# Optimization experiments

Hardware: AMD Instinct MI355X
Metric: run time of the kernel (lower is better)

## Reference

```python
import jax, jax.numpy as jnp
import numpy as np
from jax import lax

GUARD_CELLS = 80
BG_CELLS = 80
ALPHA = 1.8
CFAR_UNITS = 1 + 2 * GUARD_CELLS + 2 * BG_CELLS          # 321
GUARD_UNITS = 2 * GUARD_CELLS + 1                         # 161
BG_AREA = CFAR_UNITS ** 2 - GUARD_UNITS ** 2              # background ring cell count
FRONT_DIV = (GUARD_UNITS ** 2) * ALPHA


def box_sum(x, k):
    """Same-padded KxK box sum over NCHW x (C=1), via separable 1D convs.

    Mathematically identical to a Conv2d with all-ones KxK kernel, zero bias,
    padding (k-1)//2 -- but O(N*K) instead of O(N*K^2).
    """
    p = (k - 1) // 2
    kh = jnp.ones((1, 1, k, 1), x.dtype)  # OIHW
    kw = jnp.ones((1, 1, 1, k), x.dtype)
    y = lax.conv_general_dilated(x, kh, window_strides=(1, 1), padding=[(p, p), (0, 0)])
    y = lax.conv_general_dilated(y, kw, window_strides=(1, 1), padding=[(0, 0), (p, p)])
    return y


def setup_inputs() -> dict:
    key = jax.random.key(0)
    x = jax.random.uniform(key, (4, 1, 1024, 1024), dtype=jnp.float32)
    return {"x": x}


def reference(x) -> jnp.ndarray:
    allsum = box_sum(x, CFAR_UNITS)            # conv1: 321x321 ones box
    front = box_sum(x, GUARD_UNITS)            # conv2: 161x161 ones box
    back = (allsum - front) / jnp.float32(BG_AREA)     # div1: 1x1 conv = scale
    front = front / jnp.float32(FRONT_DIV)             # div2: 1x1 conv = scale
    return front / back
```

## Files before the change

### kernel.cpp

```cpp
#include <hip/hip_runtime.h>
#include <hip/hip_bf16.h>


#define IMG 4
#define H 1024
#define W 1024
#define SEGR 8
#define NSEG 128
#define PADL 164
#define PADR 164
#define ROWLEN (PADL + W + PADR)

__global__ __launch_bounds__(256, 4) void hbv_kernel(const float* __restrict__ x,
                                                     float* __restrict__ g161,
                                                     float* __restrict__ g321,
                                                     float* __restrict__ Btot) {
    __shared__ float P[4][ROWLEN];
    __shared__ float Hx[4][W];
    const int wave = threadIdx.x >> 6;
    const int lane = threadIdx.x & 63;
    const int q    = threadIdx.x;
    const int blk  = blockIdx.x;
    const size_t rowbase = (size_t)blk << 3;

    float4 acc1 = make_float4(0.f, 0.f, 0.f, 0.f);
    float4 acc3 = make_float4(0.f, 0.f, 0.f, 0.f);

#pragma unroll
    for (int ch = 0; ch < 2; ++ch) {
        const size_t row = rowbase + (ch << 2) + wave;
        {
            const float4* xr = reinterpret_cast<const float4*>(x + row * W);
            float v[16];
            float4 a0 = xr[(lane << 2) + 0];
            float4 a1 = xr[(lane << 2) + 1];
            float4 a2 = xr[(lane << 2) + 2];
            float4 a3 = xr[(lane << 2) + 3];
            v[0]=a0.x; v[1]=a0.y; v[2]=a0.z; v[3]=a0.w;
            v[4]=a1.x; v[5]=a1.y; v[6]=a1.z; v[7]=a1.w;
            v[8]=a2.x; v[9]=a2.y; v[10]=a2.z; v[11]=a2.w;
            v[12]=a3.x; v[13]=a3.y; v[14]=a3.z; v[15]=a3.w;
            float s = 0.f;
#pragma unroll
            for (int j = 0; j < 16; ++j) { s += v[j]; v[j] = s; }
            float t = s;
#pragma unroll
            for (int d = 1; d < 64; d <<= 1) {
                float u = __shfl_up(t, d, 64);
                if (lane >= d) t += u;
            }
            const float off = t - s;
#pragma unroll
            for (int j = 0; j < 16; ++j) v[j] += off;
            const float tot = __shfl(t, 63, 64);

            float* rowP = P[wave];
            float4* Pr = reinterpret_cast<float4*>(rowP + PADL);
            Pr[(lane << 2) + 0] = make_float4(v[0], v[1], v[2], v[3]);
            Pr[(lane << 2) + 1] = make_float4(v[4], v[5], v[6], v[7]);
            Pr[(lane << 2) + 2] = make_float4(v[8], v[9], v[10], v[11]);
            Pr[(lane << 2) + 3] = make_float4(v[12], v[13], v[14], v[15]);
            float4* Pz = reinterpret_cast<float4*>(rowP);
            if (lane < 41) {
                Pz[lane]       = make_float4(0.f, 0.f, 0.f, 0.f);
                Pz[297 + lane] = make_float4(tot, tot, tot, tot);
            }
        }
        const float* Pw = &P[wave][PADL];

#pragma unroll
        for (int k = 0; k < 16; ++k) {
            const int c = lane + (k << 6);
            Hx[wave][c] = Pw[c + 80] - Pw[c - 81];
        }
        __syncthreads();
        {
            float* o = g161 + (rowbase + (ch << 2)) * W;
            const float4* Hf = reinterpret_cast<const float4*>(Hx);
#pragma unroll
            for (int r = 0; r < 4; ++r) {
                float4 h = Hf[(r << 8) + q];
                acc1.x += h.x; acc1.y += h.y; acc1.z += h.z; acc1.w += h.w;
                reinterpret_cast<float4*>(o + (size_t)r * W)[q] = acc1;
            }
        }
        __syncthreads();
#pragma unroll
        for (int k = 0; k < 16; ++k) {
            const int c = lane + (k << 6);
            Hx[wave][c] = Pw[c + 160] - Pw[c - 161];
        }
        __syncthreads();
        {
            float* o = g321 + (rowbase + (ch << 2)) * W;
            const float4* Hf = reinterpret_cast<const float4*>(Hx);
#pragma unroll
            for (int r = 0; r < 4; ++r) {
                float4 h = Hf[(r << 8) + q];
                acc3.x += h.x; acc3.y += h.y; acc3.z += h.z; acc3.w += h.w;
                reinterpret_cast<float4*>(o + (size_t)r * W)[q] = acc3;
            }
        }
        __syncthreads();
    }

    const int img = blk >> 7;
    const int seg = blk & 127;
    float4* bt = reinterpret_cast<float4*>(Btot);
    bt[((size_t)img << 15)         + (seg << 8) + q] = acc1;
    bt[((size_t)(IMG + img) << 15) + (seg << 8) + q] = acc3;
}

__global__ __launch_bounds__(256) void segscan_kernel(const float* __restrict__ Btot,
                                                      float* __restrict__ SP) {
    __shared__ float T[4][64];
    const int wave = threadIdx.x >> 6;
    const int lane = threadIdx.x & 63;
    const int bi   = blockIdx.x >> 4;
    const int col  = ((blockIdx.x & 15) << 6) + lane;
    const size_t base = ((size_t)bi << 17) + ((size_t)(wave << 5) << 10) + col;

    float v[32];
#pragma unroll
    for (int s = 0; s < 32; ++s) v[s] = Btot[base + ((size_t)s << 10)];
    float run = 0.f;
#pragma unroll
    for (int s = 0; s < 32; ++s) { const float t = v[s]; v[s] = run; run += t; }
    T[wave][lane] = run;
    __syncthreads();
    float off = 0.f;
    for (int w = 0; w < wave; ++w) off += T[w][lane];
#pragma unroll
    for (int s = 0; s < 32; ++s) SP[base + ((size_t)s << 10)] = v[s] + off;
}

__global__ __launch_bounds__(512) void final_kernel(const float* __restrict__ g161,
                                                    const float* __restrict__ g321,
                                                    const float* __restrict__ SP,
                                                    float* __restrict__ out) {
    const int img = blockIdx.x >> 9;
    const int r   = ((blockIdx.x & 511) << 1) + (threadIdx.x >> 8);
    const int c4  = threadIdx.x & 255;

    const float4* P1 = reinterpret_cast<const float4*>(g161 + ((size_t)img << 20));
    const float4* P3 = reinterpret_cast<const float4*>(g321 + ((size_t)img << 20));
    const float4* SP1 = reinterpret_cast<const float4*>(SP) + ((size_t)img << 15);
    const float4* SP3 = reinterpret_cast<const float4*>(SP) + ((size_t)(IMG + img) << 15);

    const int hi1 = min(r + 80, H - 1),  lo1 = r - 81;
    const int hi3 = min(r + 160, H - 1), lo3 = r - 161;

    float4 f  = P1[((size_t)hi1 << 8) + c4];
    float4 fs = SP1[(((size_t)hi1 >> 3) << 8) + c4];
    float fx = f.x + fs.x, fy = f.y + fs.y, fz = f.z + fs.z, fw = f.w + fs.w;
    if (lo1 >= 0) {
        float4 g  = P1[((size_t)lo1 << 8) + c4];
        float4 gs = SP1[(((size_t)lo1 >> 3) << 8) + c4];
        fx -= g.x + gs.x; fy -= g.y + gs.y; fz -= g.z + gs.z; fw -= g.w + gs.w;
    }
    float4 a  = P3[((size_t)hi3 << 8) + c4];
    float4 as = SP3[(((size_t)hi3 >> 3) << 8) + c4];
    float ax = a.x + as.x, ay = a.y + as.y, az = a.z + as.z, aw = a.w + as.w;
    if (lo3 >= 0) {
        float4 g  = P3[((size_t)lo3 << 8) + c4];
        float4 gs = SP3[(((size_t)lo3 >> 3) << 8) + c4];
        ax -= g.x + gs.x; ay -= g.y + gs.y; az -= g.z + gs.z; aw -= g.w + gs.w;
    }

    const float SCALE = (float)(77120.0 / 46657.8);
    float4 o;
    o.x = SCALE * fx * __builtin_amdgcn_rcpf(ax - fx);
    o.y = SCALE * fy * __builtin_amdgcn_rcpf(ay - fy);
    o.z = SCALE * fz * __builtin_amdgcn_rcpf(az - fz);
    o.w = SCALE * fw * __builtin_amdgcn_rcpf(aw - fw);
    reinterpret_cast<float4*>(out + ((size_t)img << 20) + ((size_t)r << 10))[c4] = o;
}

extern "C" void kernel_launch(void* const* d_in, const int* in_sizes, int n_in,
                              void* d_out, int out_size, void* d_ws, size_t ws_size,
                              hipStream_t stream) {
    const float* x = (const float*)d_in[0];
    float* outp = (float*)d_out;
    float* g161 = (float*)d_ws;
    float* g321 = g161 + (size_t)IMG * H * W;
    float* Btot = g321 + (size_t)IMG * H * W;
    float* SPb  = Btot + (size_t)2 * IMG * NSEG * W;

    hbv_kernel<<<dim3(IMG * NSEG), dim3(256), 0, stream>>>(x, g161, g321, Btot);
    segscan_kernel<<<dim3(128), dim3(256), 0, stream>>>(Btot, SPb);
    final_kernel<<<dim3(IMG * (H / 2)), dim3(512), 0, stream>>>(g161, g321, SPb, outp);
}
```

Baseline: 90.37 us.

## Shrink row segments to 4 and fuse horizontal diff with vertical accumulation

Each block now handles 4 rows instead of 8, giving 1024 blocks. Each thread reads the prefix rows straight from shared memory and accumulates both box widths in one pass, which removes the Hx staging buffer and most of the barriers. The segment scan now covers twice as many segments with 64 values per thread and writes its result back into Btot in place, dropping the separate SP buffer. In exchange the scan kernel does more work and uses more registers, global stores become scalar rather than float4, and the shared-memory reads are unaligned scalar loads.

```diff
diff --git a/kernel.cpp b/kernel.cpp
--- a/kernel.cpp
+++ b/kernel.cpp
@@ -5,133 +5,111 @@
 #define IMG 4
 #define H 1024
 #define W 1024
-#define SEGR 8
-#define NSEG 128
+#define SEGR 4
+#define NSEG 256
 #define PADL 164
 #define PADR 164
 #define ROWLEN (PADL + W + PADR)
 
-__global__ __launch_bounds__(256, 4) void hbv_kernel(const float* __restrict__ x,
-                                                     float* __restrict__ g161,
-                                                     float* __restrict__ g321,
-                                                     float* __restrict__ Btot) {
+__global__ __launch_bounds__(256) void hbv_kernel(const float* __restrict__ x,
+                                                  float* __restrict__ g161,
+                                                  float* __restrict__ g321,
+                                                  float* __restrict__ Btot) {
     __shared__ float P[4][ROWLEN];
-    __shared__ float Hx[4][W];
     const int wave = threadIdx.x >> 6;
     const int lane = threadIdx.x & 63;
-    const int q    = threadIdx.x;
+    const int tid  = threadIdx.x;
     const int blk  = blockIdx.x;
-    const size_t rowbase = (size_t)blk << 3;
+    const size_t rowbase = (size_t)blk << 2;
 
-    float4 acc1 = make_float4(0.f, 0.f, 0.f, 0.f);
-    float4 acc3 = make_float4(0.f, 0.f, 0.f, 0.f);
+    {
+        const size_t row = rowbase + wave;
+        const float4* xr = reinterpret_cast<const float4*>(x + row * W);
+        float v[16];
+        float4 a0 = xr[(lane << 2) + 0];
+        float4 a1 = xr[(lane << 2) + 1];
+        float4 a2 = xr[(lane << 2) + 2];
+        float4 a3 = xr[(lane << 2) + 3];
+        v[0]=a0.x; v[1]=a0.y; v[2]=a0.z; v[3]=a0.w;
+        v[4]=a1.x; v[5]=a1.y; v[6]=a1.z; v[7]=a1.w;
+        v[8]=a2.x; v[9]=a2.y; v[10]=a2.z; v[11]=a2.w;
+        v[12]=a3.x; v[13]=a3.y; v[14]=a3.z; v[15]=a3.w;
+        float s = 0.f;
+#pragma unroll
+        for (int j = 0; j < 16; ++j) { s += v[j]; v[j] = s; }
+        float t = s;
+#pragma unroll
+        for (int d = 1; d < 64; d <<= 1) {
+            float u = __shfl_up(t, d, 64);
+            if (lane >= d) t += u;
+        }
+        const float off = t - s;
+#pragma unroll
+        for (int j = 0; j < 16; ++j) v[j] += off;
+        const float tot = __shfl(t, 63, 64);
 
+        float* rowP = P[wave];
+        float4* Pr = reinterpret_cast<float4*>(rowP + PADL);
+        Pr[(lane << 2) + 0] = make_float4(v[0], v[1], v[2], v[3]);
+        Pr[(lane << 2) + 1] = make_float4(v[4], v[5], v[6], v[7]);
+        Pr[(lane << 2) + 2] = make_float4(v[8], v[9], v[10], v[11]);
+        Pr[(lane << 2) + 3] = make_float4(v[12], v[13], v[14], v[15]);
+        float4* Pz = reinterpret_cast<float4*>(rowP);
+        if (lane < 41) {
+            Pz[lane]       = make_float4(0.f, 0.f, 0.f, 0.f);
+            Pz[297 + lane] = make_float4(tot, tot, tot, tot);
+        }
+    }
+    __syncthreads();
+
+    float acc1[4] = {0.f, 0.f, 0.f, 0.f};
+    float acc3[4] = {0.f, 0.f, 0.f, 0.f};
 #pragma unroll
-    for (int ch = 0; ch < 2; ++ch) {
-        const size_t row = rowbase + (ch << 2) + wave;
-        {
-            const float4* xr = reinterpret_cast<const float4*>(x + row * W);
-            float v[16];
-            float4 a0 = xr[(lane << 2) + 0];
-            float4 a1 = xr[(lane << 2) + 1];
-            float4 a2 = xr[(lane << 2) + 2];
-            float4 a3 = xr[(lane << 2) + 3];
-            v[0]=a0.x; v[1]=a0.y; v[2]=a0.z; v[3]=a0.w;
-            v[4]=a1.x; v[5]=a1.y; v[6]=a1.z; v[7]=a1.w;
-            v[8]=a2.x; v[9]=a2.y; v[10]=a2.z; v[11]=a2.w;
-            v[12]=a3.x; v[13]=a3.y; v[14]=a3.z; v[15]=a3.w;
-            float s = 0.f;
+    for (int rr = 0; rr < SEGR; ++rr) {
+        const float* Pr = &P[rr][PADL];
+        float* o1 = g161 + (rowbase + rr) * W;
+        float* o3 = g321 + (rowbase + rr) * W;
 #pragma unroll
-            for (int j = 0; j < 16; ++j) { s += v[j]; v[j] = s; }
-            float t = s;
-#pragma unroll
-            for (int d = 1; d < 64; d <<= 1) {
-                float u = __shfl_up(t, d, 64);
-                if (lane >= d) t += u;
-            }
-            const float off = t - s;
-#pragma unroll
-            for (int j = 0; j < 16; ++j) v[j] += off;
-            const float tot = __shfl(t, 63, 64);
-
-            float* rowP = P[wave];
-            float4* Pr = reinterpret_cast<float4*>(rowP + PADL);
-            Pr[(lane << 2) + 0] = make_float4(v[0], v[1], v[2], v[3]);
-            Pr[(lane << 2) + 1] = make_float4(v[4], v[5], v[6], v[7]);
-            Pr[(lane << 2) + 2] = make_float4(v[8], v[9], v[10], v[11]);
-            Pr[(lane << 2) + 3] = make_float4(v[12], v[13], v[14], v[15]);
-            float4* Pz = reinterpret_cast<float4*>(rowP);
-            if (lane < 41) {
-                Pz[lane]       = make_float4(0.f, 0.f, 0.f, 0.f);
-                Pz[297 + lane] = make_float4(tot, tot, tot, tot);
-            }
+        for (int j = 0; j < 4; ++j) {
+            const int c = tid + (j << 8);
+            acc1[j] += Pr[c + 80]  - Pr[c - 81];
+            acc3[j] += Pr[c + 160] - Pr[c - 161];
+            o1[c] = acc1[j];
+            o3[c] = acc3[j];
         }
-        const float* Pw = &P[wave][PADL];
-
-#pragma unroll
-        for (int k = 0; k < 16; ++k) {
-            const int c = lane + (k << 6);
-            Hx[wave][c] = Pw[c + 80] - Pw[c - 81];
-        }
-        __syncthreads();
-        {
-            float* o = g161 + (rowbase + (ch << 2)) * W;
-            const float4* Hf = reinterpret_cast<const float4*>(Hx);
-#pragma unroll
-            for (int r = 0; r < 4; ++r) {
-                float4 h = Hf[(r << 8) + q];
-                acc1.x += h.x; acc1.y += h.y; acc1.z += h.z; acc1.w += h.w;
-                reinterpret_cast<float4*>(o + (size_t)r * W)[q] = acc1;
-            }
-        }
-        __syncthreads();
-#pragma unroll
-        for (int k = 0; k < 16; ++k) {
-            const int c = lane + (k << 6);
-            Hx[wave][c] = Pw[c + 160] - Pw[c - 161];
-        }
-        __syncthreads();
-        {
-            float* o = g321 + (rowbase + (ch << 2)) * W;
-            const float4* Hf = reinterpret_cast<const float4*>(Hx);
-#pragma unroll
-            for (int r = 0; r < 4; ++r) {
-                float4 h = Hf[(r << 8) + q];
-                acc3.x += h.x; acc3.y += h.y; acc3.z += h.z; acc3.w += h.w;
-                reinterpret_cast<float4*>(o + (size_t)r * W)[q] = acc3;
-            }
-        }
-        __syncthreads();
     }
 
-    const int img = blk >> 7;
-    const int seg = blk & 127;
-    float4* bt = reinterpret_cast<float4*>(Btot);
-    bt[((size_t)img << 15)         + (seg << 8) + q] = acc1;
-    bt[((size_t)(IMG + img) << 15) + (seg << 8) + q] = acc3;
+    const int img = blk >> 8;
+    const int seg = blk & 255;
+    float* bt1 = Btot + ((size_t)img << 18)         + ((size_t)seg << 10);
+    float* bt3 = Btot + ((size_t)(IMG + img) << 18) + ((size_t)seg << 10);
+#pragma unroll
+    for (int j = 0; j < 4; ++j) {
+        bt1[tid + (j << 8)] = acc1[j];
+        bt3[tid + (j << 8)] = acc3[j];
+    }
 }
 
-__global__ __launch_bounds__(256) void segscan_kernel(const float* __restrict__ Btot,
-                                                      float* __restrict__ SP) {
+__global__ __launch_bounds__(256) void segscan_kernel(float* __restrict__ Btot) {
     __shared__ float T[4][64];
     const int wave = threadIdx.x >> 6;
     const int lane = threadIdx.x & 63;
     const int bi   = blockIdx.x >> 4;
     const int col  = ((blockIdx.x & 15) << 6) + lane;
-    const size_t base = ((size_t)bi << 17) + ((size_t)(wave << 5) << 10) + col;
+    const size_t base = ((size_t)bi << 18) + ((size_t)(wave << 6) << 10) + col;
 
-    float v[32];
+    float v[64];
 #pragma unroll
-    for (int s = 0; s < 32; ++s) v[s] = Btot[base + ((size_t)s << 10)];
+    for (int s = 0; s < 64; ++s) v[s] = Btot[base + ((size_t)s << 10)];
     float run = 0.f;
 #pragma unroll
-    for (int s = 0; s < 32; ++s) { const float t = v[s]; v[s] = run; run += t; }
+    for (int s = 0; s < 64; ++s) { const float t = v[s]; v[s] = run; run += t; }
     T[wave][lane] = run;
     __syncthreads();
     float off = 0.f;
     for (int w = 0; w < wave; ++w) off += T[w][lane];
 #pragma unroll
-    for (int s = 0; s < 32; ++s) SP[base + ((size_t)s << 10)] = v[s] + off;
+    for (int s = 0; s < 64; ++s) Btot[base + ((size_t)s << 10)] = v[s] + off;
 }
 
 __global__ __launch_bounds__(512) void final_kernel(const float* __restrict__ g161,
@@ -144,26 +122,26 @@
 
     const float4* P1 = reinterpret_cast<const float4*>(g161 + ((size_t)img << 20));
     const float4* P3 = reinterpret_cast<const float4*>(g321 + ((size_t)img << 20));
-    const float4* SP1 = reinterpret_cast<const float4*>(SP) + ((size_t)img << 15);
-    const float4* SP3 = reinterpret_cast<const float4*>(SP) + ((size_t)(IMG + img) << 15);
+    const float4* SP1 = reinterpret_cast<const float4*>(SP) + ((size_t)img << 16);
+    const float4* SP3 = reinterpret_cast<const float4*>(SP) + ((size_t)(IMG + img) << 16);
 
     const int hi1 = min(r + 80, H - 1),  lo1 = r - 81;
     const int hi3 = min(r + 160, H - 1), lo3 = r - 161;
 
     float4 f  = P1[((size_t)hi1 << 8) + c4];
-    float4 fs = SP1[(((size_t)hi1 >> 3) << 8) + c4];
+    float4 fs = SP1[(((size_t)hi1 >> 2) << 8) + c4];
     float fx = f.x + fs.x, fy = f.y + fs.y, fz = f.z + fs.z, fw = f.w + fs.w;
     if (lo1 >= 0) {
         float4 g  = P1[((size_t)lo1 << 8) + c4];
-        float4 gs = SP1[(((size_t)lo1 >> 3) << 8) + c4];
+        float4 gs = SP1[(((size_t)lo1 >> 2) << 8) + c4];
         fx -= g.x + gs.x; fy -= g.y + gs.y; fz -= g.z + gs.z; fw -= g.w + gs.w;
     }
     float4 a  = P3[((size_t)hi3 << 8) + c4];
-    float4 as = SP3[(((size_t)hi3 >> 3) << 8) + c4];
+    float4 as = SP3[(((size_t)hi3 >> 2) << 8) + c4];
     float ax = a.x + as.x, ay = a.y + as.y, az = a.z + as.z, aw = a.w + as.w;
     if (lo3 >= 0) {
         float4 g  = P3[((size_t)lo3 << 8) + c4];
-        float4 gs = SP3[(((size_t)lo3 >> 3) << 8) + c4];
+        float4 gs = SP3[(((size_t)lo3 >> 2) << 8) + c4];
         ax -= g.x + gs.x; ay -= g.y + gs.y; az -= g.z + gs.z; aw -= g.w + gs.w;
     }
 
@@ -184,9 +162,8 @@
     float* g161 = (float*)d_ws;
     float* g321 = g161 + (size_t)IMG * H * W;
     float* Btot = g321 + (size_t)IMG * H * W;
-    float* SPb  = Btot + (size_t)2 * IMG * NSEG * W;
 
     hbv_kernel<<<dim3(IMG * NSEG), dim3(256), 0, stream>>>(x, g161, g321, Btot);
-    segscan_kernel<<<dim3(128), dim3(256), 0, stream>>>(Btot, SPb);
-    final_kernel<<<dim3(IMG * (H / 2)), dim3(512), 0, stream>>>(g161, g321, SPb, outp);
+    segscan_kernel<<<dim3(128), dim3(256), 0, stream>>>(Btot);
+    final_kernel<<<dim3(IMG * (H / 2)), dim3(512), 0, stream>>>(g161, g321, Btot, outp);
 }
```

Result: no change. 91.61 us (+1.4%).
